# Kernel tuning notes

Measured on AMD Instinct MI355X. Metric: run time of the kernel, lower is better.

Reference implementation:

```python
import jax, jax.numpy as jnp
import numpy as np

N_NODES = 100000


def sage_conv(x, edge_index, Wl, Wr, b):
    # PyG SAGEConv(aggr='mean'): out = lin_l(mean_{j in N(i)} x_j) + lin_r(x_i)
    src, dst = edge_index[0], edge_index[1]
    msg = x[src]                                    # [E, d] gather
    agg = jax.ops.segment_sum(msg, dst, num_segments=N_NODES)
    cnt = jax.ops.segment_sum(jnp.ones((src.shape[0],), dtype=x.dtype), dst,
                              num_segments=N_NODES)
    mean = agg / jnp.maximum(cnt, 1.0)[:, None]     # isolated nodes -> 0
    return mean @ Wl + x @ Wr + b


def setup_inputs() -> dict:
    key = jax.random.key(0)
    ks = jax.random.split(key, 7)
    N, E, d_in, d_hid, d_out = N_NODES, 1000000, 64, 128, 64
    x = jax.random.normal(ks[0], (N, d_in), dtype=jnp.float32)
    W1l = jax.random.normal(ks[1], (d_in, d_hid), dtype=jnp.float32) / np.sqrt(d_in)
    W1r = jax.random.normal(ks[2], (d_in, d_hid), dtype=jnp.float32) / np.sqrt(d_in)
    b1 = jnp.zeros((d_hid,), dtype=jnp.float32)
    W2l = jax.random.normal(ks[3], (d_hid, d_out), dtype=jnp.float32) / np.sqrt(d_hid)
    W2r = jax.random.normal(ks[4], (d_hid, d_out), dtype=jnp.float32) / np.sqrt(d_hid)
    b2 = jnp.zeros((d_out,), dtype=jnp.float32)
    edge_index = jax.random.randint(ks[5], (2, E), 0, N, dtype=jnp.int64)
    return {"x": x, "W1l": W1l, "W1r": W1r, "b1": b1,
            "W2l": W2l, "W2r": W2r, "b2": b2, "edge_index": edge_index}


def reference(x, W1l, W1r, b1, W2l, W2r, b2, edge_index):
    h = jax.nn.relu(sage_conv(x, edge_index, W1l, W1r, b1))
    out = sage_conv(h, edge_index, W2l, W2r, b2)
    return out
```

## Files before the change

### kernel.cpp

```cpp
#include <hip/hip_runtime.h>

#define N_NODES 100000
#define N_EDGES 1000000
#define DEG_CAP 64
#define OVF_CAP 4096
#define SPILL_CAP 4096

#define BKT_SH 8
#define BKT_NODES 256
#define NBKT 392
#define BKT_CAP 4096
#define BIN_CHUNK 4096
#define FIFO_CAP 32

typedef __attribute__((ext_vector_type(8))) short bf16x8;
typedef __attribute__((ext_vector_type(4))) float f32x4;

__device__ __forceinline__ unsigned short f2bf(float f) {
    unsigned u = __float_as_uint(f);
    return (unsigned short)((u + 0x7FFF + ((u >> 16) & 1)) >> 16);
}
__device__ __forceinline__ float bf2f(unsigned short b) {
    return __uint_as_float(((unsigned)b) << 16);
}
__device__ __forceinline__ float bflo(unsigned u) {
    return __uint_as_float(u << 16);
}
__device__ __forceinline__ float bfhi(unsigned u) {
    return __uint_as_float(u & 0xffff0000u);
}
__device__ __forceinline__ void split_rbf(float f, unsigned short& ho,
                                          unsigned short& lo) {
    unsigned short hb = f2bf(f);
    ho = hb;
    lo = f2bf(f - bf2f(hb));
}


__global__ __launch_bounds__(256) void prep_kernel(
        const float4* __restrict__ x4,
        ushort4* __restrict__ xh4, ushort4* __restrict__ xl4,
        const float* __restrict__ W1l, const float* __restrict__ W1r,
        const float* __restrict__ W2l, const float* __restrict__ W2r,
        short* __restrict__ Bf1, short* __restrict__ Bf2,
        int4* __restrict__ gcur4, int* __restrict__ ovfc,
        int* __restrict__ spillc) {
    int i = blockIdx.x * blockDim.x + threadIdx.x;
    if (i < 128) gcur4[i] = make_int4(0, 0, 0, 0);
    if (i == 0) { *ovfc = 0; *spillc = 0; }
    if (i < 32768) {
        int g = i >> 14;
        int e = i & 16383;
        int k = e >> 7;
        int n = e & 127;
        float v;
        if (g == 0) v = (k < 64) ? W1l[k * 128 + n] : W1r[(k - 64) * 128 + n];
        else        v = (n < 64) ? W2l[k * 64 + n]  : W2r[k * 64 + (n - 64)];
        unsigned short hb, lb;
        split_rbf(v, hb, lb);
        int c = n >> 4, kc = k >> 5;
        int lane = (((k >> 3) & 3) << 4) | (n & 15);
        int j = k & 7;
        short* base = g ? Bf2 : Bf1;
        base[((c * 4 + kc) * 2 + 0) * 512 + lane * 8 + j] = (short)hb;
        base[((c * 4 + kc) * 2 + 1) * 512 + lane * 8 + j] = (short)lb;
    }
    if (i < N_NODES * 16) {
        float4 v = x4[i];
        ushort4 oh, ol;
        split_rbf(v.x, oh.x, ol.x);
        split_rbf(v.y, oh.y, ol.y);
        split_rbf(v.z, oh.z, ol.z);
        split_rbf(v.w, oh.w, ol.w);
        xh4[i] = oh;
        xl4[i] = ol;
    }
}

__global__ __launch_bounds__(256) void bin_kernel(
        const int* __restrict__ ei, unsigned* __restrict__ rec,
        int* __restrict__ gcur, int* __restrict__ spillc,
        int2* __restrict__ spill) {
    __shared__ int lcnt[NBKT];
    __shared__ unsigned fifo[NBKT * FIFO_CAP];
    for (int i = threadIdx.x; i < NBKT; i += 256) lcnt[i] = 0;
    __syncthreads();
    int base = blockIdx.x * BIN_CHUNK;
    int end = base + BIN_CHUNK;
    if (end > N_EDGES) end = N_EDGES;
    for (int e = base + threadIdx.x; e < end; e += 256) {
        int s = ei[e];
        int d = ei[N_EDGES + e];
        int b = d >> BKT_SH;
        unsigned r = ((unsigned)s << BKT_SH) | (unsigned)(d & (BKT_NODES - 1));
        int pos = atomicAdd(&lcnt[b], 1);
        if (pos < FIFO_CAP) {
            fifo[b * FIFO_CAP + pos] = r;
        } else {
            int o = atomicAdd(spillc, 1);
            if (o < SPILL_CAP) spill[o] = make_int2(s, d);
        }
    }
    __syncthreads();
    for (int b = threadIdx.x; b < NBKT; b += 256) {
        int cnt = lcnt[b];
        if (cnt > FIFO_CAP) cnt = FIFO_CAP;
        if (cnt == 0) continue;
        int gb = atomicAdd(&gcur[b], cnt);
        for (int k = 0; k < cnt; ++k) {
            int g = gb + k;
            unsigned r = fifo[b * FIFO_CAP + k];
            if (g < BKT_CAP) {
                rec[b * BKT_CAP + g] = r;
            } else {
                int o = atomicAdd(spillc, 1);
                if (o < SPILL_CAP)
                    spill[o] = make_int2((int)(r >> BKT_SH),
                                         (b << BKT_SH) | (int)(r & (BKT_NODES - 1)));
            }
        }
    }
}

__global__ __launch_bounds__(256) void build_kernel(
        const unsigned* __restrict__ rec, const int* __restrict__ gcur,
        const int2* __restrict__ spill, const int* __restrict__ spillc,
        int* __restrict__ counts, int* __restrict__ slots,
        int* __restrict__ ovfc, int* __restrict__ ovf) {
    __shared__ int lcnt[BKT_NODES];
    __shared__ int lslots[BKT_NODES * DEG_CAP];
    int b = blockIdx.x;
    for (int i = threadIdx.x; i < BKT_NODES; i += 256) lcnt[i] = 0;
    __syncthreads();
    int n = gcur[b];
    if (n > BKT_CAP) n = BKT_CAP;
    for (int i = threadIdx.x; i < n; i += 256) {
        unsigned r = rec[b * BKT_CAP + i];
        int dlo = (int)(r & (BKT_NODES - 1));
        int src = (int)(r >> BKT_SH);
        int pos = atomicAdd(&lcnt[dlo], 1);
        if (pos < DEG_CAP) {
            lslots[dlo * DEG_CAP + pos] = src;
        } else {
            int o = atomicAdd(ovfc, 1);
            if (o < OVF_CAP) {
                ovf[o * 2] = src;
                ovf[o * 2 + 1] = (b << BKT_SH) | dlo;
            }
        }
    }
    int ns = *spillc;
    if (ns > SPILL_CAP) ns = SPILL_CAP;
    for (int i = threadIdx.x; i < ns; i += 256) {
        int2 e = spill[i];
        if ((e.y >> BKT_SH) == b) {
            int dlo = e.y & (BKT_NODES - 1);
            int pos = atomicAdd(&lcnt[dlo], 1);
            if (pos < DEG_CAP) {
                lslots[dlo * DEG_CAP + pos] = e.x;
            } else {
                int o = atomicAdd(ovfc, 1);
                if (o < OVF_CAP) { ovf[o * 2] = e.x; ovf[o * 2 + 1] = e.y; }
            }
        }
    }
    __syncthreads();
    int nodeBase = b << BKT_SH;
    for (int i = threadIdx.x; i < BKT_NODES; i += 256)
        counts[nodeBase + i] = lcnt[i];
    const int4* ls4 = (const int4*)lslots;
    int4* gs4 = (int4*)(slots + nodeBase * DEG_CAP);
    for (int i = threadIdx.x; i < BKT_NODES * DEG_CAP / 4; i += 256)
        gs4[i] = ls4[i];
}

__global__ __launch_bounds__(256) void gather_bf_kernel(
        const unsigned short* __restrict__ feat, const int* __restrict__ counts,
        const int* __restrict__ slots,
        unsigned short* __restrict__ mh, unsigned short* __restrict__ ml) {
    int node = blockIdx.x * 16 + (threadIdx.x >> 4);
    int t = threadIdx.x & 15;
    if (node >= N_NODES) return;
    int deg = counts[node];
    int dcap = min(deg, DEG_CAP);
    const int gbase = threadIdx.x & 48;
    float a0 = 0.f, a1 = 0.f, a2 = 0.f, a3 = 0.f;
    for (int phase = 0; phase * 16 < dcap; ++phase) {
        int ids16 = slots[node * DEG_CAP + phase * 16 + t];
        int lim = min(dcap - phase * 16, 16);
        int j = 0;
        for (; j + 4 <= lim; j += 4) {
            int s0 = __shfl(ids16, gbase | (j + 0));
            int s1 = __shfl(ids16, gbase | (j + 1));
            int s2 = __shfl(ids16, gbase | (j + 2));
            int s3 = __shfl(ids16, gbase | (j + 3));
            uint2 u0 = *(const uint2*)(feat + s0 * 64 + t * 4);
            uint2 u1 = *(const uint2*)(feat + s1 * 64 + t * 4);
            uint2 u2 = *(const uint2*)(feat + s2 * 64 + t * 4);
            uint2 u3 = *(const uint2*)(feat + s3 * 64 + t * 4);
            a0 += bflo(u0.x) + bflo(u1.x) + bflo(u2.x) + bflo(u3.x);
            a1 += bfhi(u0.x) + bfhi(u1.x) + bfhi(u2.x) + bfhi(u3.x);
            a2 += bflo(u0.y) + bflo(u1.y) + bflo(u2.y) + bflo(u3.y);
            a3 += bfhi(u0.y) + bfhi(u1.y) + bfhi(u2.y) + bfhi(u3.y);
        }
        for (; j < lim; ++j) {
            int s = __shfl(ids16, gbase | j);
            uint2 u = *(const uint2*)(feat + s * 64 + t * 4);
            a0 += bflo(u.x);
            a1 += bfhi(u.x);
            a2 += bflo(u.y);
            a3 += bfhi(u.y);
        }
    }
    float inv = 1.0f / fmaxf((float)deg, 1.0f);
    ushort4 oh, ol;
    split_rbf(a0 * inv, oh.x, ol.x);
    split_rbf(a1 * inv, oh.y, ol.y);
    split_rbf(a2 * inv, oh.z, ol.z);
    split_rbf(a3 * inv, oh.w, ol.w);
    *(ushort4*)&mh[node * 64 + t * 4] = oh;
    *(ushort4*)&ml[node * 64 + t * 4] = ol;
}

__global__ __launch_bounds__(256) void mlp_fused_kernel(
        const unsigned short* __restrict__ mh, const unsigned short* __restrict__ ml,
        const unsigned short* __restrict__ xh, const unsigned short* __restrict__ xl,
        const float* __restrict__ x,
        const short* __restrict__ Bf1, const float* __restrict__ b1,
        const short* __restrict__ Bf2, const float* __restrict__ b2,
        const int* __restrict__ ovf, const int* __restrict__ ovfc,
        const int* __restrict__ counts,
        unsigned short* __restrict__ p_bf_out, float* __restrict__ q) {
    __shared__ unsigned short h_lds[128][136];
    const int w = threadIdx.x >> 6;
    const int l = threadIdx.x & 63;
    const int lane15 = l & 15;
    const int quad = l >> 4;
    const int rowBase = blockIdx.x * 128;

    {
        int n = *ovfc;
        if (n > OVF_CAP) n = OVF_CAP;
        if (n > 0) {
            for (int idx = 0; idx < n; ++idx) {
                int d = ovf[idx * 2 + 1];
                if (d >= rowBase && d < rowBase + 128) {
                    if (threadIdx.x < 64) {
                        int s = ovf[idx * 2];
                        int t = threadIdx.x;
                        float inv = 1.0f / fmaxf((float)counts[d], 1.0f);
                        float m = bf2f(mh[d * 64 + t]) + bf2f(ml[d * 64 + t])
                                + x[s * 64 + t] * inv;
                        unsigned short hb, lb;
                        split_rbf(m, hb, lb);
                        ((unsigned short*)mh)[d * 64 + t] = hb;
                        ((unsigned short*)ml)[d * 64 + t] = lb;
                    }
                    __syncthreads();
                }
            }
            __syncthreads();
        }
    }

    {
        bf16x8 bh[2][4], bl[2][4];
#pragma unroll
        for (int ci = 0; ci < 2; ++ci) {
            const int c = 2 * w + ci;
#pragma unroll
            for (int kc = 0; kc < 4; ++kc) {
                const short* bp = Bf1 + ((c * 4 + kc) * 2) * 512 + l * 8;
                bh[ci][kc] = *(const bf16x8*)bp;
                bl[ci][kc] = *(const bf16x8*)(bp + 512);
            }
        }
        float bias[2];
#pragma unroll
        for (int ci = 0; ci < 2; ++ci) bias[ci] = b1[(2 * w + ci) * 16 + lane15];

#pragma unroll
        for (int rt = 0; rt < 8; ++rt) {
            const int row = rowBase + rt * 16 + lane15;
            const bool rv = row < N_NODES;
            const bf16x8 zz = {0, 0, 0, 0, 0, 0, 0, 0};

            bf16x8 ah[4], al[4];
#pragma unroll
            for (int kc = 0; kc < 4; ++kc) {
                if (rv) {
                    const int off = (kc < 2)
                        ? row * 64 + kc * 32 + quad * 8
                        : row * 64 + (kc - 2) * 32 + quad * 8;
                    const unsigned short* ph = (kc < 2) ? (mh + off) : (xh + off);
                    const unsigned short* pl = (kc < 2) ? (ml + off) : (xl + off);
                    ah[kc] = *(const bf16x8*)ph;
                    al[kc] = *(const bf16x8*)pl;
                } else {
                    ah[kc] = zz;
                    al[kc] = zz;
                }
            }

            f32x4 acc[2] = {(f32x4){0.f, 0.f, 0.f, 0.f}, (f32x4){0.f, 0.f, 0.f, 0.f}};
#pragma unroll
            for (int kc = 0; kc < 4; ++kc) {
#pragma unroll
                for (int ci = 0; ci < 2; ++ci) {
                    acc[ci] = __builtin_amdgcn_mfma_f32_16x16x32_bf16(ah[kc], bh[ci][kc], acc[ci], 0, 0, 0);
                    acc[ci] = __builtin_amdgcn_mfma_f32_16x16x32_bf16(al[kc], bh[ci][kc], acc[ci], 0, 0, 0);
                    acc[ci] = __builtin_amdgcn_mfma_f32_16x16x32_bf16(ah[kc], bl[ci][kc], acc[ci], 0, 0, 0);
                }
            }

            const int rloc = rt * 16 + quad * 4;
#pragma unroll
            for (int ci = 0; ci < 2; ++ci) {
                const int col = (2 * w + ci) * 16 + lane15;
#pragma unroll
                for (int i = 0; i < 4; ++i)
                    h_lds[rloc + i][col] =
                        f2bf(fmaxf(acc[ci][i] + bias[ci], 0.f));
            }
        }
    }
    __syncthreads();

    {
        bf16x8 bh[2][4], bl[2][4];
#pragma unroll
        for (int ci = 0; ci < 2; ++ci) {
            const int c = 2 * w + ci;
#pragma unroll
            for (int kc = 0; kc < 4; ++kc) {
                const short* bp = Bf2 + ((c * 4 + kc) * 2) * 512 + l * 8;
                bh[ci][kc] = *(const bf16x8*)bp;
                bl[ci][kc] = *(const bf16x8*)(bp + 512);
            }
        }
        float bias[2];
#pragma unroll
        for (int ci = 0; ci < 2; ++ci) {
            const int c = 2 * w + ci;
            bias[ci] = (c >= 4) ? b2[(c - 4) * 16 + lane15] : 0.f;
        }

#pragma unroll
        for (int rt = 0; rt < 8; ++rt) {
            bf16x8 ah[4];
#pragma unroll
            for (int kc = 0; kc < 4; ++kc)
                ah[kc] = *(const bf16x8*)&h_lds[rt * 16 + lane15][kc * 32 + quad * 8];

            f32x4 acc[2] = {(f32x4){0.f, 0.f, 0.f, 0.f}, (f32x4){0.f, 0.f, 0.f, 0.f}};
#pragma unroll
            for (int kc = 0; kc < 4; ++kc) {
#pragma unroll
                for (int ci = 0; ci < 2; ++ci) {
                    acc[ci] = __builtin_amdgcn_mfma_f32_16x16x32_bf16(ah[kc], bh[ci][kc], acc[ci], 0, 0, 0);
                    acc[ci] = __builtin_amdgcn_mfma_f32_16x16x32_bf16(ah[kc], bl[ci][kc], acc[ci], 0, 0, 0);
                }
            }

            const int rb = rowBase + rt * 16 + quad * 4;
#pragma unroll
            for (int ci = 0; ci < 2; ++ci) {
                const int c = 2 * w + ci;
                if (c < 4) {
#pragma unroll
                    for (int i = 0; i < 4; ++i) {
                        int r = rb + i;
                        if (r < N_NODES)
                            p_bf_out[r * 64 + c * 16 + lane15] = f2bf(acc[ci][i]);
                    }
                } else {
#pragma unroll
                    for (int i = 0; i < 4; ++i) {
                        int r = rb + i;
                        if (r < N_NODES)
                            q[r * 64 + (c - 4) * 16 + lane15] = acc[ci][i] + bias[ci];
                    }
                }
            }
        }
    }
}

__global__ __launch_bounds__(256) void gather_final_kernel(
        const unsigned short* __restrict__ p, const int* __restrict__ counts,
        const int* __restrict__ slots, const float* __restrict__ q,
        const int* __restrict__ ovf, const int* __restrict__ ovfc,
        float* __restrict__ out) {
    int node = blockIdx.x * 16 + (threadIdx.x >> 4);
    int t = threadIdx.x & 15;
    if (node >= N_NODES) return;
    int deg = counts[node];
    int dcap = min(deg, DEG_CAP);
    const int gbase = threadIdx.x & 48;
    float a0 = 0.f, a1 = 0.f, a2 = 0.f, a3 = 0.f;
    for (int phase = 0; phase * 16 < dcap; ++phase) {
        int ids16 = slots[node * DEG_CAP + phase * 16 + t];
        int lim = min(dcap - phase * 16, 16);
        int j = 0;
        for (; j + 4 <= lim; j += 4) {
            int s0 = __shfl(ids16, gbase | (j + 0));
            int s1 = __shfl(ids16, gbase | (j + 1));
            int s2 = __shfl(ids16, gbase | (j + 2));
            int s3 = __shfl(ids16, gbase | (j + 3));
            uint2 u0 = *(const uint2*)(p + s0 * 64 + t * 4);
            uint2 u1 = *(const uint2*)(p + s1 * 64 + t * 4);
            uint2 u2 = *(const uint2*)(p + s2 * 64 + t * 4);
            uint2 u3 = *(const uint2*)(p + s3 * 64 + t * 4);
            a0 += bflo(u0.x) + bflo(u1.x) + bflo(u2.x) + bflo(u3.x);
            a1 += bfhi(u0.x) + bfhi(u1.x) + bfhi(u2.x) + bfhi(u3.x);
            a2 += bflo(u0.y) + bflo(u1.y) + bflo(u2.y) + bflo(u3.y);
            a3 += bfhi(u0.y) + bfhi(u1.y) + bfhi(u2.y) + bfhi(u3.y);
        }
        for (; j < lim; ++j) {
            int s = __shfl(ids16, gbase | j);
            uint2 u = *(const uint2*)(p + s * 64 + t * 4);
            a0 += bflo(u.x);
            a1 += bfhi(u.x);
            a2 += bflo(u.y);
            a3 += bfhi(u.y);
        }
    }
    int n = *ovfc;
    if (n > OVF_CAP) n = OVF_CAP;
    for (int idx = 0; idx < n; ++idx) {
        if (ovf[idx * 2 + 1] == node) {
            int s = ovf[idx * 2];
            uint2 u = *(const uint2*)(p + s * 64 + t * 4);
            a0 += bflo(u.x);
            a1 += bfhi(u.x);
            a2 += bflo(u.y);
            a3 += bfhi(u.y);
        }
    }
    float inv = 1.0f / fmaxf((float)deg, 1.0f);
    float4 qv = *(const float4*)&q[node * 64 + t * 4];
    *(float4*)&out[node * 64 + t * 4] =
        make_float4(a0 * inv + qv.x, a1 * inv + qv.y,
                    a2 * inv + qv.z, a3 * inv + qv.w);
}

extern "C" void kernel_launch(void* const* d_in, const int* in_sizes, int n_in,
                              void* d_out, int out_size, void* d_ws, size_t ws_size,
                              hipStream_t stream) {
    const float* x   = (const float*)d_in[0];
    const float* W1l = (const float*)d_in[1];
    const float* W1r = (const float*)d_in[2];
    const float* b1  = (const float*)d_in[3];
    const float* W2l = (const float*)d_in[4];
    const float* W2r = (const float*)d_in[5];
    const float* b2  = (const float*)d_in[6];
    const int*   ei  = (const int*)d_in[7];

    int*   wsi      = (int*)d_ws;
    float* wsf      = (float*)d_ws;
    int*   counts   = wsi;
    int*   ovfc     = wsi + 100352;
    int*   spillc   = wsi + 100353;
    int*   gcur     = wsi + 100416;
    int*   ovf      = wsi + 100928;
    int2*  spill    = (int2*)(wsi + 109120);
    short* Bf1      = (short*)(wsi + 117312);
    short* Bf2      = (short*)(wsi + 133696);
    int*   slots    = wsi + 150080;
    unsigned* rec   = (unsigned*)(wsi + 6572608);
    unsigned short* xh = (unsigned short*)(wsi + 8178240);
    unsigned short* xl = (unsigned short*)(wsi + 11378240);
    unsigned short* mh = (unsigned short*)(wsi + 14578240);
    unsigned short* ml = (unsigned short*)(wsi + 17778240);
    unsigned short* p_bf = (unsigned short*)(wsi + 20978240);
    float* q        = wsf + 24178240;
    float* out      = (float*)d_out;

    prep_kernel<<<(N_NODES * 16 + 255) / 256, 256, 0, stream>>>(
        (const float4*)x, (ushort4*)xh, (ushort4*)xl, W1l, W1r, W2l, W2r,
        Bf1, Bf2, (int4*)gcur, ovfc, spillc);

    bin_kernel<<<(N_EDGES + BIN_CHUNK - 1) / BIN_CHUNK, 256, 0, stream>>>(
        ei, rec, gcur, spillc, spill);
    build_kernel<<<NBKT, 256, 0, stream>>>(
        rec, gcur, spill, spillc, counts, slots, ovfc, ovf);

    gather_bf_kernel<<<(N_NODES + 15) / 16, 256, 0, stream>>>(
        xh, counts, slots, mh, ml);

    mlp_fused_kernel<<<(N_NODES + 127) / 128, 256, 0, stream>>>(
        mh, ml, xh, xl, x, Bf1, b1, Bf2, b2, ovf, ovfc, counts, p_bf, q);

    gather_final_kernel<<<(N_NODES + 15) / 16, 256, 0, stream>>>(
        p_bf, counts, slots, q, ovf, ovfc, out);
}
```

Baseline: 215.2 us.

## Fuse first-layer neighbor mean gather into the MLP kernel via LDS

Removes the separate gather kernel and computes each node's neighbor mean inside the fused MLP kernel, storing the hi/lo bf16 split in shared memory instead of writing and re-reading mh/ml in global memory. Each wave handles 32 rows, one thread per row with 4 quad-lanes splitting the 64 features, and loops over that row's slots. The overflow-edge correction now scans the whole overflow list per row rather than per block. It also double-buffers the x-row loads across row tiles. The risk is that one thread per row with serial neighbour loads gives less parallelism and more divergence than the old 16-lanes-per-node gather, and it uses more LDS, which can lower occupancy.

```diff
diff --git a/kernel.cpp b/kernel.cpp
--- a/kernel.cpp
+++ b/kernel.cpp
@@ -174,63 +174,16 @@
         gs4[i] = ls4[i];
 }
 
-__global__ __launch_bounds__(256) void gather_bf_kernel(
-        const unsigned short* __restrict__ feat, const int* __restrict__ counts,
-        const int* __restrict__ slots,
-        unsigned short* __restrict__ mh, unsigned short* __restrict__ ml) {
-    int node = blockIdx.x * 16 + (threadIdx.x >> 4);
-    int t = threadIdx.x & 15;
-    if (node >= N_NODES) return;
-    int deg = counts[node];
-    int dcap = min(deg, DEG_CAP);
-    const int gbase = threadIdx.x & 48;
-    float a0 = 0.f, a1 = 0.f, a2 = 0.f, a3 = 0.f;
-    for (int phase = 0; phase * 16 < dcap; ++phase) {
-        int ids16 = slots[node * DEG_CAP + phase * 16 + t];
-        int lim = min(dcap - phase * 16, 16);
-        int j = 0;
-        for (; j + 4 <= lim; j += 4) {
-            int s0 = __shfl(ids16, gbase | (j + 0));
-            int s1 = __shfl(ids16, gbase | (j + 1));
-            int s2 = __shfl(ids16, gbase | (j + 2));
-            int s3 = __shfl(ids16, gbase | (j + 3));
-            uint2 u0 = *(const uint2*)(feat + s0 * 64 + t * 4);
-            uint2 u1 = *(const uint2*)(feat + s1 * 64 + t * 4);
-            uint2 u2 = *(const uint2*)(feat + s2 * 64 + t * 4);
-            uint2 u3 = *(const uint2*)(feat + s3 * 64 + t * 4);
-            a0 += bflo(u0.x) + bflo(u1.x) + bflo(u2.x) + bflo(u3.x);
-            a1 += bfhi(u0.x) + bfhi(u1.x) + bfhi(u2.x) + bfhi(u3.x);
-            a2 += bflo(u0.y) + bflo(u1.y) + bflo(u2.y) + bflo(u3.y);
-            a3 += bfhi(u0.y) + bfhi(u1.y) + bfhi(u2.y) + bfhi(u3.y);
-        }
-        for (; j < lim; ++j) {
-            int s = __shfl(ids16, gbase | j);
-            uint2 u = *(const uint2*)(feat + s * 64 + t * 4);
-            a0 += bflo(u.x);
-            a1 += bfhi(u.x);
-            a2 += bflo(u.y);
-            a3 += bfhi(u.y);
-        }
-    }
-    float inv = 1.0f / fmaxf((float)deg, 1.0f);
-    ushort4 oh, ol;
-    split_rbf(a0 * inv, oh.x, ol.x);
-    split_rbf(a1 * inv, oh.y, ol.y);
-    split_rbf(a2 * inv, oh.z, ol.z);
-    split_rbf(a3 * inv, oh.w, ol.w);
-    *(ushort4*)&mh[node * 64 + t * 4] = oh;
-    *(ushort4*)&ml[node * 64 + t * 4] = ol;
-}
-
 __global__ __launch_bounds__(256) void mlp_fused_kernel(
-        const unsigned short* __restrict__ mh, const unsigned short* __restrict__ ml,
         const unsigned short* __restrict__ xh, const unsigned short* __restrict__ xl,
         const float* __restrict__ x,
+        const int* __restrict__ counts, const int* __restrict__ slots,
         const short* __restrict__ Bf1, const float* __restrict__ b1,
         const short* __restrict__ Bf2, const float* __restrict__ b2,
         const int* __restrict__ ovf, const int* __restrict__ ovfc,
-        const int* __restrict__ counts,
         unsigned short* __restrict__ p_bf_out, float* __restrict__ q) {
+    __shared__ unsigned short mean_h[128][72];
+    __shared__ unsigned short mean_l[128][72];
     __shared__ unsigned short h_lds[128][136];
     const int w = threadIdx.x >> 6;
     const int l = threadIdx.x & 63;
@@ -239,29 +192,87 @@
     const int rowBase = blockIdx.x * 128;
 
     {
-        int n = *ovfc;
-        if (n > OVF_CAP) n = OVF_CAP;
-        if (n > 0) {
-            for (int idx = 0; idx < n; ++idx) {
-                int d = ovf[idx * 2 + 1];
-                if (d >= rowBase && d < rowBase + 128) {
-                    if (threadIdx.x < 64) {
-                        int s = ovf[idx * 2];
-                        int t = threadIdx.x;
-                        float inv = 1.0f / fmaxf((float)counts[d], 1.0f);
-                        float m = bf2f(mh[d * 64 + t]) + bf2f(ml[d * 64 + t])
-                                + x[s * 64 + t] * inv;
-                        unsigned short hb, lb;
-                        split_rbf(m, hb, lb);
-                        ((unsigned short*)mh)[d * 64 + t] = hb;
-                        ((unsigned short*)ml)[d * 64 + t] = lb;
+        int n_ovf = *ovfc;
+        if (n_ovf > OVF_CAP) n_ovf = OVF_CAP;
+        const int fb0 = quad * 8;
+        const int fb1 = 32 + quad * 8;
+#pragma unroll
+        for (int pass = 0; pass < 2; ++pass) {
+            const int rloc = w * 32 + pass * 16 + lane15;
+            const int row = rowBase + rloc;
+            const bool rv = row < N_NODES;
+            int deg = rv ? counts[row] : 0;
+            int dcap = min(deg, DEG_CAP);
+            float s[16];
+#pragma unroll
+            for (int i = 0; i < 16; ++i) s[i] = 0.f;
+            int j = 0;
+            for (; j + 2 <= dcap; j += 2) {
+                int id0 = slots[row * DEG_CAP + j];
+                int id1 = slots[row * DEG_CAP + j + 1];
+                uint4 a0 = *(const uint4*)(xh + id0 * 64 + fb0);
+                uint4 b0 = *(const uint4*)(xh + id0 * 64 + fb1);
+                uint4 a1 = *(const uint4*)(xh + id1 * 64 + fb0);
+                uint4 b1v = *(const uint4*)(xh + id1 * 64 + fb1);
+                s[0] += bflo(a0.x) + bflo(a1.x);  s[1] += bfhi(a0.x) + bfhi(a1.x);
+                s[2] += bflo(a0.y) + bflo(a1.y);  s[3] += bfhi(a0.y) + bfhi(a1.y);
+                s[4] += bflo(a0.z) + bflo(a1.z);  s[5] += bfhi(a0.z) + bfhi(a1.z);
+                s[6] += bflo(a0.w) + bflo(a1.w);  s[7] += bfhi(a0.w) + bfhi(a1.w);
+                s[8]  += bflo(b0.x) + bflo(b1v.x); s[9]  += bfhi(b0.x) + bfhi(b1v.x);
+                s[10] += bflo(b0.y) + bflo(b1v.y); s[11] += bfhi(b0.y) + bfhi(b1v.y);
+                s[12] += bflo(b0.z) + bflo(b1v.z); s[13] += bfhi(b0.z) + bfhi(b1v.z);
+                s[14] += bflo(b0.w) + bflo(b1v.w); s[15] += bfhi(b0.w) + bfhi(b1v.w);
+            }
+            if (j < dcap) {
+                int id0 = slots[row * DEG_CAP + j];
+                uint4 a0 = *(const uint4*)(xh + id0 * 64 + fb0);
+                uint4 b0 = *(const uint4*)(xh + id0 * 64 + fb1);
+                s[0] += bflo(a0.x);  s[1] += bfhi(a0.x);
+                s[2] += bflo(a0.y);  s[3] += bfhi(a0.y);
+                s[4] += bflo(a0.z);  s[5] += bfhi(a0.z);
+                s[6] += bflo(a0.w);  s[7] += bfhi(a0.w);
+                s[8]  += bflo(b0.x); s[9]  += bfhi(b0.x);
+                s[10] += bflo(b0.y); s[11] += bfhi(b0.y);
+                s[12] += bflo(b0.z); s[13] += bfhi(b0.z);
+                s[14] += bflo(b0.w); s[15] += bfhi(b0.w);
+            }
+            float inv = 1.0f / fmaxf((float)deg, 1.0f);
+            float m[16];
+#pragma unroll
+            for (int i = 0; i < 16; ++i) m[i] = s[i] * inv;
+            for (int idx = 0; idx < n_ovf; ++idx) {
+                if (ovf[idx * 2 + 1] == row) {
+                    int sx = ovf[idx * 2];
+#pragma unroll
+                    for (int i = 0; i < 8; ++i) {
+                        m[i]     += x[sx * 64 + fb0 + i] * inv;
+                        m[8 + i] += x[sx * 64 + fb1 + i] * inv;
                     }
-                    __syncthreads();
                 }
             }
-            __syncthreads();
-        }
-    }
+            unsigned short hh[16], ll[16];
+#pragma unroll
+            for (int i = 0; i < 16; ++i) split_rbf(m[i], hh[i], ll[i]);
+            ushort4 v;
+            v.x = hh[0]; v.y = hh[1]; v.z = hh[2]; v.w = hh[3];
+            *(ushort4*)&mean_h[rloc][fb0] = v;
+            v.x = hh[4]; v.y = hh[5]; v.z = hh[6]; v.w = hh[7];
+            *(ushort4*)&mean_h[rloc][fb0 + 4] = v;
+            v.x = hh[8]; v.y = hh[9]; v.z = hh[10]; v.w = hh[11];
+            *(ushort4*)&mean_h[rloc][fb1] = v;
+            v.x = hh[12]; v.y = hh[13]; v.z = hh[14]; v.w = hh[15];
+            *(ushort4*)&mean_h[rloc][fb1 + 4] = v;
+            v.x = ll[0]; v.y = ll[1]; v.z = ll[2]; v.w = ll[3];
+            *(ushort4*)&mean_l[rloc][fb0] = v;
+            v.x = ll[4]; v.y = ll[5]; v.z = ll[6]; v.w = ll[7];
+            *(ushort4*)&mean_l[rloc][fb0 + 4] = v;
+            v.x = ll[8]; v.y = ll[9]; v.z = ll[10]; v.w = ll[11];
+            *(ushort4*)&mean_l[rloc][fb1] = v;
+            v.x = ll[12]; v.y = ll[13]; v.z = ll[14]; v.w = ll[15];
+            *(ushort4*)&mean_l[rloc][fb1 + 4] = v;
+        }
+    }
+    __syncthreads();
 
     {
         bf16x8 bh[2][4], bl[2][4];
@@ -279,30 +290,32 @@
 #pragma unroll
         for (int ci = 0; ci < 2; ++ci) bias[ci] = b1[(2 * w + ci) * 16 + lane15];
 
-#pragma unroll
-        for (int rt = 0; rt < 8; ++rt) {
+        const bf16x8 zz = {0, 0, 0, 0, 0, 0, 0, 0};
+        auto load_x = [&](int rt, bf16x8 (&xhf)[2], bf16x8 (&xlf)[2]) {
             const int row = rowBase + rt * 16 + lane15;
             const bool rv = row < N_NODES;
-            const bf16x8 zz = {0, 0, 0, 0, 0, 0, 0, 0};
-
-            bf16x8 ah[4], al[4];
-#pragma unroll
-            for (int kc = 0; kc < 4; ++kc) {
+#pragma unroll
+            for (int kk = 0; kk < 2; ++kk) {
                 if (rv) {
-                    const int off = (kc < 2)
-                        ? row * 64 + kc * 32 + quad * 8
-                        : row * 64 + (kc - 2) * 32 + quad * 8;
-                    const unsigned short* ph = (kc < 2) ? (mh + off) : (xh + off);
-                    const unsigned short* pl = (kc < 2) ? (ml + off) : (xl + off);
-                    ah[kc] = *(const bf16x8*)ph;
-                    al[kc] = *(const bf16x8*)pl;
+                    const int off = row * 64 + kk * 32 + quad * 8;
+                    xhf[kk] = *(const bf16x8*)(xh + off);
+                    xlf[kk] = *(const bf16x8*)(xl + off);
                 } else {
-                    ah[kc] = zz;
-                    al[kc] = zz;
+                    xhf[kk] = zz;
+                    xlf[kk] = zz;
                 }
             }
-
-            f32x4 acc[2] = {(f32x4){0.f, 0.f, 0.f, 0.f}, (f32x4){0.f, 0.f, 0.f, 0.f}};
+        };
+        auto compute_store = [&](bf16x8 (&xhf)[2], bf16x8 (&xlf)[2], int rt) {
+            const int rl = rt * 16 + lane15;
+            bf16x8 mh0 = *(const bf16x8*)&mean_h[rl][quad * 8];
+            bf16x8 mh1 = *(const bf16x8*)&mean_h[rl][32 + quad * 8];
+            bf16x8 ml0 = *(const bf16x8*)&mean_l[rl][quad * 8];
+            bf16x8 ml1 = *(const bf16x8*)&mean_l[rl][32 + quad * 8];
+            bf16x8 ah[4] = {mh0, mh1, xhf[0], xhf[1]};
+            bf16x8 al[4] = {ml0, ml1, xlf[0], xlf[1]};
+            f32x4 acc[2] = {(f32x4){0.f, 0.f, 0.f, 0.f},
+                            (f32x4){0.f, 0.f, 0.f, 0.f}};
 #pragma unroll
             for (int kc = 0; kc < 4; ++kc) {
 #pragma unroll
@@ -312,7 +325,6 @@
                     acc[ci] = __builtin_amdgcn_mfma_f32_16x16x32_bf16(ah[kc], bl[ci][kc], acc[ci], 0, 0, 0);
                 }
             }
-
             const int rloc = rt * 16 + quad * 4;
 #pragma unroll
             for (int ci = 0; ci < 2; ++ci) {
@@ -322,6 +334,16 @@
                     h_lds[rloc + i][col] =
                         f2bf(fmaxf(acc[ci][i] + bias[ci], 0.f));
             }
+        };
+
+        bf16x8 xhA[2], xlA[2], xhB[2], xlB[2];
+        load_x(0, xhA, xlA);
+#pragma unroll
+        for (int rt = 0; rt < 8; rt += 2) {
+            load_x(rt + 1, xhB, xlB);
+            compute_store(xhA, xlA, rt);
+            if (rt + 2 < 8) load_x(rt + 2, xhA, xlA);
+            compute_store(xhB, xlB, rt + 1);
         }
     }
     __syncthreads();
@@ -470,8 +492,6 @@
     unsigned* rec   = (unsigned*)(wsi + 6572608);
     unsigned short* xh = (unsigned short*)(wsi + 8178240);
     unsigned short* xl = (unsigned short*)(wsi + 11378240);
-    unsigned short* mh = (unsigned short*)(wsi + 14578240);
-    unsigned short* ml = (unsigned short*)(wsi + 17778240);
     unsigned short* p_bf = (unsigned short*)(wsi + 20978240);
     float* q        = wsf + 24178240;
     float* out      = (float*)d_out;
@@ -485,11 +505,8 @@
     build_kernel<<<NBKT, 256, 0, stream>>>(
         rec, gcur, spill, spillc, counts, slots, ovfc, ovf);
 
-    gather_bf_kernel<<<(N_NODES + 15) / 16, 256, 0, stream>>>(
-        xh, counts, slots, mh, ml);
-
     mlp_fused_kernel<<<(N_NODES + 127) / 128, 256, 0, stream>>>(
-        mh, ml, xh, xl, x, Bf1, b1, Bf2, b2, ovf, ovfc, counts, p_bf, q);
+        xh, xl, x, counts, slots, Bf1, b1, Bf2, b2, ovf, ovfc, p_bf, q);
 
     gather_final_kernel<<<(N_NODES + 15) / 16, 256, 0, stream>>>(
         p_bf, counts, slots, q, ovf, ovfc, out);
```

Result: no change. 212.6 us (-1.2%).
